# Optimization experiments

Measured on AMD Instinct MI355X. Metric: run time of the kernel, lower is better.

Reference implementation:

```python
import jax, jax.numpy as jnp
import numpy as np

N = 50000
E = 800000
H_IN = 64
HEADS1 = 4
NEG_SLOPE = 0.2


def gat_conv(x, W, att_src, att_dst, bias, src, dst, heads, out_ch):
    """PyG GATConv (add_self_loops=False, concat=True).
    x: [N, in]; W: [in, heads*out_ch]; att_*: [heads, out_ch]; bias: [heads*out_ch].
    """
    n = x.shape[0]
    h = (x @ W).reshape(n, heads, out_ch)                 # [N, H, C]
    a_s = jnp.einsum('nhc,hc->nh', h, att_src)            # [N, H]
    a_d = jnp.einsum('nhc,hc->nh', h, att_dst)            # [N, H]
    e = jax.nn.leaky_relu(a_s[src] + a_d[dst], NEG_SLOPE) # [E, H]
    # segment softmax over incoming edges of each destination node
    e_max = jax.ops.segment_max(e, dst, num_segments=n)
    e_exp = jnp.exp(e - e_max[dst])
    denom = jax.ops.segment_sum(e_exp, dst, num_segments=n)
    alpha = e_exp / denom[dst]                            # [E, H]
    msg = h[src] * alpha[:, :, None]                      # [E, H, C]
    out = jax.ops.segment_sum(msg, dst, num_segments=n)   # [N, H, C]
    return out.reshape(n, heads * out_ch) + bias


def setup_inputs() -> dict:
    key = jax.random.key(0)
    ks = jax.random.split(key, 10)
    x = jax.random.normal(ks[0], (N, H_IN), dtype=jnp.float32)
    edge_index = jax.random.randint(ks[1], (2, E), 0, N, dtype=jnp.int64)
    s1 = 1.0 / np.sqrt(H_IN)
    W1 = jax.random.normal(ks[2], (H_IN, HEADS1 * H_IN), dtype=jnp.float32) * s1
    att_src1 = jax.random.normal(ks[3], (HEADS1, H_IN), dtype=jnp.float32) * s1
    att_dst1 = jax.random.normal(ks[4], (HEADS1, H_IN), dtype=jnp.float32) * s1
    b1 = jnp.zeros((HEADS1 * H_IN,), dtype=jnp.float32)
    s2 = 1.0 / np.sqrt(HEADS1 * H_IN)
    W2 = jax.random.normal(ks[5], (HEADS1 * H_IN, H_IN), dtype=jnp.float32) * s2
    att_src2 = jax.random.normal(ks[6], (1, H_IN), dtype=jnp.float32) * s2
    att_dst2 = jax.random.normal(ks[7], (1, H_IN), dtype=jnp.float32) * s2
    b2 = jnp.zeros((H_IN,), dtype=jnp.float32)
    return {"x": x, "edge_index": edge_index, "W1": W1, "att_src1": att_src1,
            "att_dst1": att_dst1, "b1": b1, "W2": W2, "att_src2": att_src2,
            "att_dst2": att_dst2, "b2": b2}


def reference(x, edge_index, W1, att_src1, att_dst1, b1, W2, att_src2, att_dst2, b2):
    src, dst = edge_index[0], edge_index[1]
    h = gat_conv(x, W1, att_src1, att_dst1, b1, src, dst, HEADS1, H_IN)
    h = jax.nn.relu(h)
    out = gat_conv(h, W2, att_src2, att_dst2, b2, src, dst, 1, H_IN)
    return out
```

## Files before the change

kernel.cpp:

```cpp
#include <hip/hip_runtime.h>
#include <hip/hip_fp16.h>

#define NEG_SLOPE 0.2f
#define H_IN 64

__device__ __forceinline__ float lrelu(float v) { return v > 0.f ? v : NEG_SLOPE * v; }

__global__ __launch_bounds__(256) void zero_int2(int* __restrict__ a,
                                                 int* __restrict__ b, int n)
{
    int i = blockIdx.x * 256 + threadIdx.x;
    if (i < n) { a[i] = 0; b[i] = 0; }
}

__global__ __launch_bounds__(256) void hist_kernel(const int* __restrict__ dst,
                                                   int* __restrict__ deg, int ne)
{
    int e = blockIdx.x * 256 + threadIdx.x;
    if (e < ne) atomicAdd(&deg[dst[e]], 1);
}

__global__ __launch_bounds__(256) void block_sum(const int* __restrict__ deg,
                                                 int* __restrict__ bsum, int n)
{
    __shared__ int part[4];
    int i = blockIdx.x * 256 + threadIdx.x;
    int v = (i < n) ? deg[i] : 0;
    #pragma unroll
    for (int off = 32; off; off >>= 1) v += __shfl_down(v, off);
    int lane = threadIdx.x & 63, wv = threadIdx.x >> 6;
    if (lane == 0) part[wv] = v;
    __syncthreads();
    if (threadIdx.x == 0)
        bsum[blockIdx.x] = part[0] + part[1] + part[2] + part[3];
}

__global__ __launch_bounds__(256) void scan_bsum(const int* __restrict__ bsum,
                                                 int* __restrict__ bpre, int nb)
{
    __shared__ int sm[256];
    int t = threadIdx.x;
    int v = (t < nb) ? bsum[t] : 0;
    sm[t] = v; __syncthreads();
    for (int off = 1; off < 256; off <<= 1) {
        int y = (t >= off) ? sm[t - off] : 0;
        __syncthreads();
        if (t >= off) sm[t] += y;
        __syncthreads();
    }
    if (t < nb) bpre[t] = sm[t] - v;
}

__global__ __launch_bounds__(256) void scan_rowptr(const int* __restrict__ deg,
                                                   const int* __restrict__ bpre,
                                                   int* __restrict__ rowptr, int n)
{
    __shared__ int sm[256];
    int t = threadIdx.x;
    int i = blockIdx.x * 256 + t;
    int v = (i < n) ? deg[i] : 0;
    sm[t] = v; __syncthreads();
    for (int off = 1; off < 256; off <<= 1) {
        int y = (t >= off) ? sm[t - off] : 0;
        __syncthreads();
        if (t >= off) sm[t] += y;
        __syncthreads();
    }
    if (i < n) rowptr[i] = sm[t] - v + bpre[blockIdx.x];
}

__global__ __launch_bounds__(256) void scatter_kernel(
    const int* __restrict__ src, const int* __restrict__ dst,
    const int* __restrict__ rowptr, int* __restrict__ cursor,
    int* __restrict__ csr_src, int ne)
{
    int e = blockIdx.x * 256 + threadIdx.x;
    if (e >= ne) return;
    int t = dst[e];
    int pos = atomicAdd(&cursor[t], 1);
    csr_src[rowptr[t] + pos] = src[e];
}

__global__ __launch_bounds__(256) void micro_wa(
    const float* __restrict__ W1, const float* __restrict__ as1, const float* __restrict__ ad1,
    const float* __restrict__ W2, const float* __restrict__ as2, const float* __restrict__ ad2,
    float* __restrict__ wa1s, float* __restrict__ wa1d,
    float* __restrict__ wa2s, float* __restrict__ wa2d)
{
    int tid = threadIdx.x;
    int k = tid >> 2, h = tid & 3;
    float s = 0.f, d = 0.f;
    #pragma unroll 8
    for (int c = 0; c < 64; ++c) {
        float w = W1[k * 256 + h * 64 + c];
        s = fmaf(w, as1[h * 64 + c], s);
        d = fmaf(w, ad1[h * 64 + c], d);
    }
    wa1s[k * 4 + h] = s; wa1d[k * 4 + h] = d;
    float s2 = 0.f, d2 = 0.f;
    #pragma unroll 8
    for (int c = 0; c < 64; ++c) {
        float w = W2[tid * 64 + c];
        s2 = fmaf(w, as2[c], s2);
        d2 = fmaf(w, ad2[c], d2);
    }
    wa2s[tid] = s2; wa2d[tid] = d2;
}

__global__ __launch_bounds__(256) void axw1_kernel(
    const float* __restrict__ x,
    const float* __restrict__ wa1s, const float* __restrict__ wa1d,
    float* __restrict__ a_s, float* __restrict__ a_d, int n)
{
    __shared__ float ws[256], wd[256];
    int tid = threadIdx.x;
    ws[tid] = wa1s[tid]; wd[tid] = wa1d[tid];
    __syncthreads();
    int row = blockIdx.x * 256 + tid;
    if (row >= n) return;
    const float4* xv = (const float4*)(x + (size_t)row * 64);
    float aS[4] = {0, 0, 0, 0}, aD[4] = {0, 0, 0, 0};
    #pragma unroll
    for (int k4 = 0; k4 < 16; ++k4) {
        float4 q = xv[k4];
        float xe[4] = {q.x, q.y, q.z, q.w};
        #pragma unroll
        for (int e = 0; e < 4; ++e) {
            int k = k4 * 4 + e;
            #pragma unroll
            for (int h = 0; h < 4; ++h) {
                aS[h] = fmaf(xe[e], ws[k * 4 + h], aS[h]);
                aD[h] = fmaf(xe[e], wd[k * 4 + h], aD[h]);
            }
        }
    }
    #pragma unroll
    for (int h = 0; h < 4; ++h) {
        a_s[row * 4 + h] = aS[h];
        a_d[row * 4 + h] = aD[h];
    }
}

__global__ __launch_bounds__(256) void gemm1_kernel(
    const float* __restrict__ x, const float* __restrict__ W1,
    __half* __restrict__ h1, int n)
{
    __shared__ float w_s[64 * 256];
    int tid = threadIdx.x;
    {
        const float4* Wv = (const float4*)W1;
        float4* wv = (float4*)w_s;
        for (int i = tid; i < 4096; i += 256) wv[i] = Wv[i];
    }
    __syncthreads();
    int row0 = blockIdx.x * 16;
    for (int sub = 0; sub < 4; ++sub) {
        const float4* x0 = (const float4*)(x + (size_t)(row0 + sub * 4) * 64);
        const float4* x1 = x0 + 16;
        const float4* x2 = x0 + 32;
        const float4* x3 = x0 + 48;
        float a0 = 0.f, a1 = 0.f, a2 = 0.f, a3 = 0.f;
        #pragma unroll
        for (int k4 = 0; k4 < 16; ++k4) {
            float4 q0 = x0[k4], q1 = x1[k4], q2 = x2[k4], q3 = x3[k4];
            const float* f0 = (const float*)&q0;
            const float* f1 = (const float*)&q1;
            const float* f2 = (const float*)&q2;
            const float* f3 = (const float*)&q3;
            #pragma unroll
            for (int e = 0; e < 4; ++e) {
                float w = w_s[(k4 * 4 + e) * 256 + tid];
                a0 = fmaf(f0[e], w, a0);
                a1 = fmaf(f1[e], w, a1);
                a2 = fmaf(f2[e], w, a2);
                a3 = fmaf(f3[e], w, a3);
            }
        }
        size_t base = (size_t)(row0 + sub * 4) * 256 + tid;
        h1[base]       = __float2half(a0);
        h1[base + 256] = __float2half(a1);
        h1[base + 512] = __float2half(a2);
        h1[base + 768] = __float2half(a3);
    }
}

__global__ __launch_bounds__(256) void gemm2_kernel(
    const __half* __restrict__ xr, const float* __restrict__ W2,
    __half* __restrict__ h2, int n)
{
    __shared__ float w_s[256 * 64];
    int tid = threadIdx.x;
    {
        const float4* Wv = (const float4*)W2;
        float4* wv = (float4*)w_s;
        for (int i = tid; i < 4096; i += 256) wv[i] = Wv[i];
    }
    __syncthreads();
    int col = tid & 63, wv_ = tid >> 6;
    int row0 = blockIdx.x * 64 + wv_ * 16;
    for (int sub = 0; sub < 4; ++sub) {
        int r0 = row0 + sub * 4;
        const float4* x0 = (const float4*)(xr + (size_t)r0 * 256);
        const float4* x1 = x0 + 32;
        const float4* x2 = x0 + 64;
        const float4* x3 = x0 + 96;
        float a0 = 0.f, a1 = 0.f, a2 = 0.f, a3 = 0.f;
        #pragma unroll 8
        for (int k8 = 0; k8 < 32; ++k8) {
            float4 q0 = x0[k8], q1 = x1[k8], q2 = x2[k8], q3 = x3[k8];
            const __half2* p0 = (const __half2*)&q0;
            const __half2* p1 = (const __half2*)&q1;
            const __half2* p2 = (const __half2*)&q2;
            const __half2* p3 = (const __half2*)&q3;
            #pragma unroll
            for (int e = 0; e < 4; ++e) {
                float2 g0 = __half22float2(p0[e]);
                float2 g1 = __half22float2(p1[e]);
                float2 g2 = __half22float2(p2[e]);
                float2 g3 = __half22float2(p3[e]);
                float wA = w_s[(k8 * 8 + e * 2) * 64 + col];
                float wB = w_s[(k8 * 8 + e * 2 + 1) * 64 + col];
                a0 = fmaf(g0.x, wA, a0); a0 = fmaf(g0.y, wB, a0);
                a1 = fmaf(g1.x, wA, a1); a1 = fmaf(g1.y, wB, a1);
                a2 = fmaf(g2.x, wA, a2); a2 = fmaf(g2.y, wB, a2);
                a3 = fmaf(g3.x, wA, a3); a3 = fmaf(g3.y, wB, a3);
            }
        }
        if (r0 + 3 < n) {
            size_t b = (size_t)r0 * 64 + col;
            h2[b]       = __float2half(a0);
            h2[b + 64]  = __float2half(a1);
            h2[b + 128] = __float2half(a2);
            h2[b + 192] = __float2half(a3);
        } else {
            float av[4] = {a0, a1, a2, a3};
            for (int r = 0; r < 4; ++r)
                if (r0 + r < n) h2[(size_t)(r0 + r) * 64 + col] = __float2half(av[r]);
        }
    }
}

__global__ __launch_bounds__(256) void aggr1_csr(
    const int* __restrict__ rowptr, const int* __restrict__ deg,
    const int* __restrict__ csr_src,
    const float* __restrict__ a_s, const float* __restrict__ a_d,
    const __half* __restrict__ h1, const float* __restrict__ b1,
    const float* __restrict__ wa2s, const float* __restrict__ wa2d,
    __half* __restrict__ out1r, float* __restrict__ a_s2, float* __restrict__ a_d2,
    int n)
{
    __shared__ float al[4][64];
    __shared__ int   ss[64];
    __shared__ float ev[4][128];
    __shared__ float p1[4], p2[4];
    int t = blockIdx.x;
    int tid = threadIdx.x, h = tid >> 6, lane = tid & 63;
    int row0 = rowptr[t], d = deg[t];
    float adt = a_d[t * 4 + h];
    float w2s = wa2s[tid], w2d = wa2d[tid];
    bool small = (d <= 128);

    float m = -INFINITY;
    if (small) {
        for (int i = lane; i < d; i += 64) {
            float v = lrelu(a_s[csr_src[row0 + i] * 4 + h] + adt);
            ev[h][i] = v;
            m = fmaxf(m, v);
        }
    } else {
        for (int i = lane; i < d; i += 64)
            m = fmaxf(m, lrelu(a_s[csr_src[row0 + i] * 4 + h] + adt));
    }
    #pragma unroll
    for (int off = 32; off; off >>= 1) m = fmaxf(m, __shfl_xor(m, off));

    float dsum = 0.f;
    if (small) {
        for (int i = lane; i < d; i += 64) dsum += __expf(ev[h][i] - m);
    } else {
        for (int i = lane; i < d; i += 64)
            dsum += __expf(lrelu(a_s[csr_src[row0 + i] * 4 + h] + adt) - m);
    }
    #pragma unroll
    for (int off = 32; off; off >>= 1) dsum += __shfl_xor(dsum, off);
    float inv = (d > 0) ? 1.f / dsum : 0.f;

    float acc = 0.f;
    for (int c0 = 0; c0 < d; c0 += 64) {
        int i = c0 + lane;
        float alpha = 0.f;
        if (i < d) {
            float v = small ? ev[h][i] : lrelu(a_s[csr_src[row0 + i] * 4 + h] + adt);
            alpha = __expf(v - m) * inv;
        }
        al[h][lane] = alpha;
        if (h == 0) ss[lane] = (i < d) ? csr_src[row0 + i] * 256 : 0;
        __syncthreads();
        int cl = min(64, d - c0);
        const __half* hp = h1 + tid;
        int j = 0;
        for (; j + 4 <= cl; j += 4) {
            int o0 = ss[j], o1 = ss[j + 1], o2 = ss[j + 2], o3 = ss[j + 3];
            float b0 = al[h][j], c1 = al[h][j + 1], c2 = al[h][j + 2], c3 = al[h][j + 3];
            float v0 = __half2float(hp[o0]), v1 = __half2float(hp[o1]);
            float v2 = __half2float(hp[o2]), v3 = __half2float(hp[o3]);
            acc = fmaf(b0, v0, acc);
            acc = fmaf(c1, v1, acc);
            acc = fmaf(c2, v2, acc);
            acc = fmaf(c3, v3, acc);
        }
        for (; j < cl; ++j) acc = fmaf(al[h][j], __half2float(hp[ss[j]]), acc);
        __syncthreads();
    }

    float r = fmaxf(acc + b1[tid], 0.f);
    out1r[(size_t)t * 256 + tid] = __float2half(r);
    float s2 = r * w2s, d2v = r * w2d;
    #pragma unroll
    for (int off = 32; off; off >>= 1) {
        s2  += __shfl_down(s2, off);
        d2v += __shfl_down(d2v, off);
    }
    if (lane == 0) { p1[h] = s2; p2[h] = d2v; }
    __syncthreads();
    if (tid == 0) {
        a_s2[t] = p1[0] + p1[1] + p1[2] + p1[3];
        a_d2[t] = p2[0] + p2[1] + p2[2] + p2[3];
    }
}

__global__ __launch_bounds__(256) void aggr2_csr(
    const int* __restrict__ rowptr, const int* __restrict__ deg,
    const int* __restrict__ csr_src,
    const float* __restrict__ a_s, const float* __restrict__ a_d,
    const __half* __restrict__ h2, const float* __restrict__ b2,
    float* __restrict__ dout, int n)
{
    __shared__ float ev2[4][128];
    __shared__ float al2[4][64];
    __shared__ int   ss2[4][64];
    int wv = threadIdx.x >> 6, lane = threadIdx.x & 63;
    int t = blockIdx.x * 4 + wv;
    if (t >= n) return;
    int row0 = rowptr[t], d = deg[t];
    float adt = a_d[t];
    bool small = (d <= 128);

    float m = -INFINITY;
    if (small) {
        for (int i = lane; i < d; i += 64) {
            float v = lrelu(a_s[csr_src[row0 + i]] + adt);
            ev2[wv][i] = v;
            m = fmaxf(m, v);
        }
    } else {
        for (int i = lane; i < d; i += 64)
            m = fmaxf(m, lrelu(a_s[csr_src[row0 + i]] + adt));
    }
    #pragma unroll
    for (int off = 32; off; off >>= 1) m = fmaxf(m, __shfl_xor(m, off));

    float dsum = 0.f;
    if (small) {
        for (int i = lane; i < d; i += 64) dsum += __expf(ev2[wv][i] - m);
    } else {
        for (int i = lane; i < d; i += 64)
            dsum += __expf(lrelu(a_s[csr_src[row0 + i]] + adt) - m);
    }
    #pragma unroll
    for (int off = 32; off; off >>= 1) dsum += __shfl_xor(dsum, off);
    float inv = (d > 0) ? 1.f / dsum : 0.f;

    float acc = 0.f;
    for (int c0 = 0; c0 < d; c0 += 64) {
        int i = c0 + lane;
        float alpha = 0.f; int so = 0;
        if (i < d) {
            int s = csr_src[row0 + i];
            so = s * 64;
            float v = small ? ev2[wv][i] : lrelu(a_s[s] + adt);
            alpha = __expf(v - m) * inv;
        }
        al2[wv][lane] = alpha;
        ss2[wv][lane] = so;
        int cl = min(64, d - c0);
        const __half* hp = h2 + lane;
        int j = 0;
        for (; j + 4 <= cl; j += 4) {
            int o0 = ss2[wv][j], o1 = ss2[wv][j + 1], o2 = ss2[wv][j + 2], o3 = ss2[wv][j + 3];
            float b0 = al2[wv][j], c1 = al2[wv][j + 1], c2 = al2[wv][j + 2], c3 = al2[wv][j + 3];
            float v0 = __half2float(hp[o0]), v1 = __half2float(hp[o1]);
            float v2 = __half2float(hp[o2]), v3 = __half2float(hp[o3]);
            acc = fmaf(b0, v0, acc);
            acc = fmaf(c1, v1, acc);
            acc = fmaf(c2, v2, acc);
            acc = fmaf(c3, v3, acc);
        }
        for (; j < cl; ++j) acc = fmaf(al2[wv][j], __half2float(hp[ss2[wv][j]]), acc);
    }
    dout[(size_t)t * 64 + lane] = acc + b2[lane];
}

extern "C" void kernel_launch(void* const* d_in, const int* in_sizes, int n_in,
                              void* d_out, int out_size, void* d_ws, size_t ws_size,
                              hipStream_t stream)
{
    const float* x    = (const float*)d_in[0];
    const int*   ei   = (const int*)d_in[1];
    const float* W1   = (const float*)d_in[2];
    const float* as1  = (const float*)d_in[3];
    const float* ad1  = (const float*)d_in[4];
    const float* b1   = (const float*)d_in[5];
    const float* W2   = (const float*)d_in[6];
    const float* as2  = (const float*)d_in[7];
    const float* ad2  = (const float*)d_in[8];
    const float* b2   = (const float*)d_in[9];
    float* dout = (float*)d_out;

    const int n  = in_sizes[0] / H_IN;
    const int ne = in_sizes[1] / 2;
    const int* src = ei;
    const int* dst = ei + ne;
    const int NB = (n + 255) / 256;

    float* ws = (float*)d_ws;
    __half* h1h   = (__half*)ws;
    __half* out1r = h1h + (size_t)n * 256;
    float* fbase  = ws + (size_t)n * 256;
    float* a_s1   = fbase;
    float* a_d1   = a_s1   + (size_t)n * 4;
    float* a_s2   = a_d1   + (size_t)n * 4;
    float* a_d2   = a_s2   + (size_t)n;
    float* wa1s   = a_d2   + (size_t)n;
    float* wa1d   = wa1s + 256;
    float* wa2s   = wa1d + 256;
    float* wa2d   = wa2s + 256;
    int*   deg    = (int*)(wa2d + 256);
    int*   rowptr = deg + n;
    int*   csr    = rowptr + n;
    int*   bsum   = csr + ne;
    int*   bpre   = bsum + NB;
    int*   cursor = (int*)h1h;
    __half* h2h   = h1h;

    micro_wa<<<1, 256, 0, stream>>>(W1, as1, ad1, W2, as2, ad2, wa1s, wa1d, wa2s, wa2d);

    zero_int2<<<NB, 256, 0, stream>>>(deg, cursor, n);
    hist_kernel<<<(ne + 255) / 256, 256, 0, stream>>>(dst, deg, ne);
    block_sum<<<NB, 256, 0, stream>>>(deg, bsum, n);
    scan_bsum<<<1, 256, 0, stream>>>(bsum, bpre, NB);
    scan_rowptr<<<NB, 256, 0, stream>>>(deg, bpre, rowptr, n);
    scatter_kernel<<<(ne + 255) / 256, 256, 0, stream>>>(src, dst, rowptr, cursor, csr, ne);

    axw1_kernel<<<NB, 256, 0, stream>>>(x, wa1s, wa1d, a_s1, a_d1, n);
    gemm1_kernel<<<n / 16, 256, 0, stream>>>(x, W1, h1h, n);
    aggr1_csr<<<n, 256, 0, stream>>>(rowptr, deg, csr, a_s1, a_d1, h1h, b1,
                                     wa2s, wa2d, out1r, a_s2, a_d2, n);

    gemm2_kernel<<<(n + 63) / 64, 256, 0, stream>>>(out1r, W2, h2h, n);
    aggr2_csr<<<(n + 3) / 4, 256, 0, stream>>>(rowptr, deg, csr, a_s2, a_d2, h2h, b2, dout, n);
}
```

Baseline: 496.1 us.

## Split GEMM weight staging into K halves and vectorize aggregation gathers as half2

Both GEMM kernels now stage the weight matrix in two K-halves, halving shared memory per block so more blocks fit per CU, at the cost of an extra barrier and an extra pass over the inputs. The two aggregation kernels now gather half2 pairs instead of single halves. Each thread covers two channels and the block or wave is split into two edge-parity groups whose partial sums are merged through shared memory or a shuffle. This halves the number of gather instructions per edge and widens each load, in exchange for the combine step and more complex indexing.

```diff
diff --git a/kernel.cpp b/kernel.cpp
--- a/kernel.cpp
+++ b/kernel.cpp
@@ -145,42 +145,56 @@
     const float* __restrict__ x, const float* __restrict__ W1,
     __half* __restrict__ h1, int n)
 {
-    __shared__ float w_s[64 * 256];
+    __shared__ float w_s[32 * 256];
     int tid = threadIdx.x;
-    {
-        const float4* Wv = (const float4*)W1;
-        float4* wv = (float4*)w_s;
-        for (int i = tid; i < 4096; i += 256) wv[i] = Wv[i];
-    }
-    __syncthreads();
     int row0 = blockIdx.x * 16;
+    float acc[4][4];
+    #pragma unroll
+    for (int s = 0; s < 4; ++s)
+        #pragma unroll
+        for (int r = 0; r < 4; ++r) acc[s][r] = 0.f;
+
+    const float4* Wv = (const float4*)W1;
+    for (int kk = 0; kk < 2; ++kk) {
+        if (kk) __syncthreads();
+        {
+            float4* wv = (float4*)w_s;
+            #pragma unroll
+            for (int i = 0; i < 8; ++i)
+                wv[tid + i * 256] = Wv[kk * 2048 + tid + i * 256];
+        }
+        __syncthreads();
+        #pragma unroll
+        for (int sub = 0; sub < 4; ++sub) {
+            const float4* x0 = (const float4*)(x + (size_t)(row0 + sub * 4) * 64 + kk * 32);
+            const float4* x1 = x0 + 16;
+            const float4* x2 = x0 + 32;
+            const float4* x3 = x0 + 48;
+            #pragma unroll
+            for (int k4 = 0; k4 < 8; ++k4) {
+                float4 q0 = x0[k4], q1 = x1[k4], q2 = x2[k4], q3 = x3[k4];
+                const float* f0 = (const float*)&q0;
+                const float* f1 = (const float*)&q1;
+                const float* f2 = (const float*)&q2;
+                const float* f3 = (const float*)&q3;
+                #pragma unroll
+                for (int e = 0; e < 4; ++e) {
+                    float w = w_s[(k4 * 4 + e) * 256 + tid];
+                    acc[sub][0] = fmaf(f0[e], w, acc[sub][0]);
+                    acc[sub][1] = fmaf(f1[e], w, acc[sub][1]);
+                    acc[sub][2] = fmaf(f2[e], w, acc[sub][2]);
+                    acc[sub][3] = fmaf(f3[e], w, acc[sub][3]);
+                }
+            }
+        }
+    }
+    #pragma unroll
     for (int sub = 0; sub < 4; ++sub) {
-        const float4* x0 = (const float4*)(x + (size_t)(row0 + sub * 4) * 64);
-        const float4* x1 = x0 + 16;
-        const float4* x2 = x0 + 32;
-        const float4* x3 = x0 + 48;
-        float a0 = 0.f, a1 = 0.f, a2 = 0.f, a3 = 0.f;
-        #pragma unroll
-        for (int k4 = 0; k4 < 16; ++k4) {
-            float4 q0 = x0[k4], q1 = x1[k4], q2 = x2[k4], q3 = x3[k4];
-            const float* f0 = (const float*)&q0;
-            const float* f1 = (const float*)&q1;
-            const float* f2 = (const float*)&q2;
-            const float* f3 = (const float*)&q3;
-            #pragma unroll
-            for (int e = 0; e < 4; ++e) {
-                float w = w_s[(k4 * 4 + e) * 256 + tid];
-                a0 = fmaf(f0[e], w, a0);
-                a1 = fmaf(f1[e], w, a1);
-                a2 = fmaf(f2[e], w, a2);
-                a3 = fmaf(f3[e], w, a3);
-            }
-        }
         size_t base = (size_t)(row0 + sub * 4) * 256 + tid;
-        h1[base]       = __float2half(a0);
-        h1[base + 256] = __float2half(a1);
-        h1[base + 512] = __float2half(a2);
-        h1[base + 768] = __float2half(a3);
+        h1[base]       = __float2half(acc[sub][0]);
+        h1[base + 256] = __float2half(acc[sub][1]);
+        h1[base + 512] = __float2half(acc[sub][2]);
+        h1[base + 768] = __float2half(acc[sub][3]);
     }
 }
 
@@ -188,54 +202,68 @@
     const __half* __restrict__ xr, const float* __restrict__ W2,
     __half* __restrict__ h2, int n)
 {
-    __shared__ float w_s[256 * 64];
+    __shared__ float w_s[128 * 64];
     int tid = threadIdx.x;
-    {
-        const float4* Wv = (const float4*)W2;
-        float4* wv = (float4*)w_s;
-        for (int i = tid; i < 4096; i += 256) wv[i] = Wv[i];
-    }
-    __syncthreads();
     int col = tid & 63, wv_ = tid >> 6;
     int row0 = blockIdx.x * 64 + wv_ * 16;
+    float acc[4][4];
+    #pragma unroll
+    for (int s = 0; s < 4; ++s)
+        #pragma unroll
+        for (int r = 0; r < 4; ++r) acc[s][r] = 0.f;
+
+    const float4* Wv = (const float4*)W2;
+    for (int kk = 0; kk < 2; ++kk) {
+        if (kk) __syncthreads();
+        {
+            float4* wv = (float4*)w_s;
+            #pragma unroll
+            for (int i = 0; i < 8; ++i)
+                wv[tid + i * 256] = Wv[kk * 2048 + tid + i * 256];
+        }
+        __syncthreads();
+        #pragma unroll
+        for (int sub = 0; sub < 4; ++sub) {
+            int r0 = row0 + sub * 4;
+            const float4* x0 = (const float4*)(xr + (size_t)r0 * 256 + kk * 128);
+            const float4* x1 = x0 + 32;
+            const float4* x2 = x0 + 64;
+            const float4* x3 = x0 + 96;
+            #pragma unroll 4
+            for (int k8 = 0; k8 < 16; ++k8) {
+                float4 q0 = x0[k8], q1 = x1[k8], q2 = x2[k8], q3 = x3[k8];
+                const __half2* p0 = (const __half2*)&q0;
+                const __half2* p1 = (const __half2*)&q1;
+                const __half2* p2 = (const __half2*)&q2;
+                const __half2* p3 = (const __half2*)&q3;
+                #pragma unroll
+                for (int e = 0; e < 4; ++e) {
+                    float2 g0 = __half22float2(p0[e]);
+                    float2 g1 = __half22float2(p1[e]);
+                    float2 g2 = __half22float2(p2[e]);
+                    float2 g3 = __half22float2(p3[e]);
+                    float wA = w_s[(k8 * 8 + e * 2) * 64 + col];
+                    float wB = w_s[(k8 * 8 + e * 2 + 1) * 64 + col];
+                    acc[sub][0] = fmaf(g0.x, wA, acc[sub][0]); acc[sub][0] = fmaf(g0.y, wB, acc[sub][0]);
+                    acc[sub][1] = fmaf(g1.x, wA, acc[sub][1]); acc[sub][1] = fmaf(g1.y, wB, acc[sub][1]);
+                    acc[sub][2] = fmaf(g2.x, wA, acc[sub][2]); acc[sub][2] = fmaf(g2.y, wB, acc[sub][2]);
+                    acc[sub][3] = fmaf(g3.x, wA, acc[sub][3]); acc[sub][3] = fmaf(g3.y, wB, acc[sub][3]);
+                }
+            }
+        }
+    }
+    #pragma unroll
     for (int sub = 0; sub < 4; ++sub) {
         int r0 = row0 + sub * 4;
-        const float4* x0 = (const float4*)(xr + (size_t)r0 * 256);
-        const float4* x1 = x0 + 32;
-        const float4* x2 = x0 + 64;
-        const float4* x3 = x0 + 96;
-        float a0 = 0.f, a1 = 0.f, a2 = 0.f, a3 = 0.f;
-        #pragma unroll 8
-        for (int k8 = 0; k8 < 32; ++k8) {
-            float4 q0 = x0[k8], q1 = x1[k8], q2 = x2[k8], q3 = x3[k8];
-            const __half2* p0 = (const __half2*)&q0;
-            const __half2* p1 = (const __half2*)&q1;
-            const __half2* p2 = (const __half2*)&q2;
-            const __half2* p3 = (const __half2*)&q3;
-            #pragma unroll
-            for (int e = 0; e < 4; ++e) {
-                float2 g0 = __half22float2(p0[e]);
-                float2 g1 = __half22float2(p1[e]);
-                float2 g2 = __half22float2(p2[e]);
-                float2 g3 = __half22float2(p3[e]);
-                float wA = w_s[(k8 * 8 + e * 2) * 64 + col];
-                float wB = w_s[(k8 * 8 + e * 2 + 1) * 64 + col];
-                a0 = fmaf(g0.x, wA, a0); a0 = fmaf(g0.y, wB, a0);
-                a1 = fmaf(g1.x, wA, a1); a1 = fmaf(g1.y, wB, a1);
-                a2 = fmaf(g2.x, wA, a2); a2 = fmaf(g2.y, wB, a2);
-                a3 = fmaf(g3.x, wA, a3); a3 = fmaf(g3.y, wB, a3);
-            }
-        }
         if (r0 + 3 < n) {
             size_t b = (size_t)r0 * 64 + col;
-            h2[b]       = __float2half(a0);
-            h2[b + 64]  = __float2half(a1);
-            h2[b + 128] = __float2half(a2);
-            h2[b + 192] = __float2half(a3);
+            h2[b]       = __float2half(acc[sub][0]);
+            h2[b + 64]  = __float2half(acc[sub][1]);
+            h2[b + 128] = __float2half(acc[sub][2]);
+            h2[b + 192] = __float2half(acc[sub][3]);
         } else {
-            float av[4] = {a0, a1, a2, a3};
             for (int r = 0; r < 4; ++r)
-                if (r0 + r < n) h2[(size_t)(r0 + r) * 64 + col] = __float2half(av[r]);
+                if (r0 + r < n) h2[(size_t)(r0 + r) * 64 + col] = __float2half(acc[sub][r]);
         }
     }
 }
@@ -252,12 +280,12 @@
     __shared__ float al[4][64];
     __shared__ int   ss[64];
     __shared__ float ev[4][128];
-    __shared__ float p1[4], p2[4];
+    __shared__ float2 pm[128];
+    __shared__ float p1[2], p2[2];
     int t = blockIdx.x;
     int tid = threadIdx.x, h = tid >> 6, lane = tid & 63;
     int row0 = rowptr[t], d = deg[t];
     float adt = a_d[t * 4 + h];
-    float w2s = wa2s[tid], w2d = wa2d[tid];
     bool small = (d <= 128);
 
     float m = -INFINITY;
@@ -285,7 +313,12 @@
     for (int off = 32; off; off >>= 1) dsum += __shfl_xor(dsum, off);
     float inv = (d > 0) ? 1.f / dsum : 0.f;
 
-    float acc = 0.f;
+    int cpair = tid & 127;
+    int p = tid >> 7;
+    int hc = cpair >> 5;
+    float2 acc = make_float2(0.f, 0.f);
+    const __half2* hbase = (const __half2*)h1;
+
     for (int c0 = 0; c0 < d; c0 += 64) {
         int i = c0 + lane;
         float alpha = 0.f;
@@ -294,38 +327,49 @@
             alpha = __expf(v - m) * inv;
         }
         al[h][lane] = alpha;
-        if (h == 0) ss[lane] = (i < d) ? csr_src[row0 + i] * 256 : 0;
+        if (h == 0) ss[lane] = (i < d) ? csr_src[row0 + i] * 128 : 0;
         __syncthreads();
         int cl = min(64, d - c0);
-        const __half* hp = h1 + tid;
-        int j = 0;
-        for (; j + 4 <= cl; j += 4) {
-            int o0 = ss[j], o1 = ss[j + 1], o2 = ss[j + 2], o3 = ss[j + 3];
-            float b0 = al[h][j], c1 = al[h][j + 1], c2 = al[h][j + 2], c3 = al[h][j + 3];
-            float v0 = __half2float(hp[o0]), v1 = __half2float(hp[o1]);
-            float v2 = __half2float(hp[o2]), v3 = __half2float(hp[o3]);
-            acc = fmaf(b0, v0, acc);
-            acc = fmaf(c1, v1, acc);
-            acc = fmaf(c2, v2, acc);
-            acc = fmaf(c3, v3, acc);
-        }
-        for (; j < cl; ++j) acc = fmaf(al[h][j], __half2float(hp[ss[j]]), acc);
-        __syncthreads();
-    }
-
-    float r = fmaxf(acc + b1[tid], 0.f);
-    out1r[(size_t)t * 256 + tid] = __float2half(r);
-    float s2 = r * w2s, d2v = r * w2d;
-    #pragma unroll
-    for (int off = 32; off; off >>= 1) {
-        s2  += __shfl_down(s2, off);
-        d2v += __shfl_down(d2v, off);
-    }
-    if (lane == 0) { p1[h] = s2; p2[h] = d2v; }
+        int j = p;
+        for (; j + 2 < cl; j += 4) {
+            float a0 = al[hc][j];
+            float a1 = al[hc][j + 2];
+            float2 g0 = __half22float2(hbase[ss[j] + cpair]);
+            float2 g1 = __half22float2(hbase[ss[j + 2] + cpair]);
+            acc.x = fmaf(a0, g0.x, acc.x);
+            acc.y = fmaf(a0, g0.y, acc.y);
+            acc.x = fmaf(a1, g1.x, acc.x);
+            acc.y = fmaf(a1, g1.y, acc.y);
+        }
+        if (j < cl) {
+            float a0 = al[hc][j];
+            float2 g0 = __half22float2(hbase[ss[j] + cpair]);
+            acc.x = fmaf(a0, g0.x, acc.x);
+            acc.y = fmaf(a0, g0.y, acc.y);
+        }
+        __syncthreads();
+    }
+
+    if (p == 1) pm[cpair] = acc;
+    __syncthreads();
+    if (p == 0) {
+        float2 o = pm[cpair];
+        float r0v = fmaxf(acc.x + o.x + b1[2 * cpair], 0.f);
+        float r1v = fmaxf(acc.y + o.y + b1[2 * cpair + 1], 0.f);
+        ((__half2*)out1r)[(size_t)t * 128 + cpair] = __floats2half2_rn(r0v, r1v);
+        float s2  = r0v * wa2s[2 * cpair] + r1v * wa2s[2 * cpair + 1];
+        float d2v = r0v * wa2d[2 * cpair] + r1v * wa2d[2 * cpair + 1];
+        #pragma unroll
+        for (int off = 32; off; off >>= 1) {
+            s2  += __shfl_down(s2, off);
+            d2v += __shfl_down(d2v, off);
+        }
+        if ((tid & 63) == 0) { p1[tid >> 6] = s2; p2[tid >> 6] = d2v; }
+    }
     __syncthreads();
     if (tid == 0) {
-        a_s2[t] = p1[0] + p1[1] + p1[2] + p1[3];
-        a_d2[t] = p2[0] + p2[1] + p2[2] + p2[3];
+        a_s2[t] = p1[0] + p1[1];
+        a_d2[t] = p2[0] + p2[1];
     }
 }
 
@@ -371,34 +415,50 @@
     for (int off = 32; off; off >>= 1) dsum += __shfl_xor(dsum, off);
     float inv = (d > 0) ? 1.f / dsum : 0.f;
 
-    float acc = 0.f;
+    int c2 = lane & 31;
+    int p = lane >> 5;
+    float2 acc = make_float2(0.f, 0.f);
+    const __half2* hbase = (const __half2*)h2;
+
     for (int c0 = 0; c0 < d; c0 += 64) {
         int i = c0 + lane;
         float alpha = 0.f; int so = 0;
         if (i < d) {
             int s = csr_src[row0 + i];
-            so = s * 64;
+            so = s * 32;
             float v = small ? ev2[wv][i] : lrelu(a_s[s] + adt);
             alpha = __expf(v - m) * inv;
         }
         al2[wv][lane] = alpha;
         ss2[wv][lane] = so;
         int cl = min(64, d - c0);
-        const __half* hp = h2 + lane;
-        int j = 0;
-        for (; j + 4 <= cl; j += 4) {
-            int o0 = ss2[wv][j], o1 = ss2[wv][j + 1], o2 = ss2[wv][j + 2], o3 = ss2[wv][j + 3];
-            float b0 = al2[wv][j], c1 = al2[wv][j + 1], c2 = al2[wv][j + 2], c3 = al2[wv][j + 3];
-            float v0 = __half2float(hp[o0]), v1 = __half2float(hp[o1]);
-            float v2 = __half2float(hp[o2]), v3 = __half2float(hp[o3]);
-            acc = fmaf(b0, v0, acc);
-            acc = fmaf(c1, v1, acc);
-            acc = fmaf(c2, v2, acc);
-            acc = fmaf(c3, v3, acc);
-        }
-        for (; j < cl; ++j) acc = fmaf(al2[wv][j], __half2float(hp[ss2[wv][j]]), acc);
-    }
-    dout[(size_t)t * 64 + lane] = acc + b2[lane];
+        int j = p;
+        for (; j + 2 < cl; j += 4) {
+            float a0 = al2[wv][j];
+            float a1 = al2[wv][j + 2];
+            float2 g0 = __half22float2(hbase[ss2[wv][j] + c2]);
+            float2 g1 = __half22float2(hbase[ss2[wv][j + 2] + c2]);
+            acc.x = fmaf(a0, g0.x, acc.x);
+            acc.y = fmaf(a0, g0.y, acc.y);
+            acc.x = fmaf(a1, g1.x, acc.x);
+            acc.y = fmaf(a1, g1.y, acc.y);
+        }
+        if (j < cl) {
+            float a0 = al2[wv][j];
+            float2 g0 = __half22float2(hbase[ss2[wv][j] + c2]);
+            acc.x = fmaf(a0, g0.x, acc.x);
+            acc.y = fmaf(a0, g0.y, acc.y);
+        }
+    }
+
+    acc.x += __shfl_down(acc.x, 32);
+    acc.y += __shfl_down(acc.y, 32);
+    if (p == 0) {
+        float2 o;
+        o.x = acc.x + b2[2 * c2];
+        o.y = acc.y + b2[2 * c2 + 1];
+        ((float2*)(dout + (size_t)t * 64))[c2] = o;
+    }
 }
 
 extern "C" void kernel_launch(void* const* d_in, const int* in_sizes, int n_in,
```

Result: faster. 443.1 us (-10.7%).
